# Performance work log

Hardware: AMD Instinct MI355X
Metric: run time of the kernel (lower is better)

## Reference

```python
import jax, jax.numpy as jnp
import numpy as np

# hyperparameters (from init_kwargs / repo defaults)
AMP_COEF = 1.0
ARG_COEF = 1.0
SSIM_COEF = 1.0
BETA = 1.0
STFT_COEF = 1e-4
EPS = 1e-8
STFT_F = 12
STFT_S = 4


def _gauss_kernel(size=11, sigma=1.5):
    x = jnp.arange(size, dtype=jnp.float32) - (size - 1) / 2.0
    g = jnp.exp(-0.5 * (x / sigma) ** 2)
    k = jnp.outer(g, g)
    return k / jnp.sum(k)


def _depthwise_filter(img, k):
    # img: [B,H,W,C]; 11x11 gaussian, VALID padding, depthwise (per-channel)
    c = img.shape[-1]
    kern = jnp.tile(k[:, :, None, None], (1, 1, 1, c))  # HWIO, I=1, O=C
    return jax.lax.conv_general_dilated(
        img, kern, (1, 1), 'VALID',
        dimension_numbers=('NHWC', 'HWIO', 'NHWC'),
        feature_group_count=c)


def ssim(x, y, max_val=1.0):
    # faithful to tf.image.ssim defaults: filter 11, sigma 1.5, k1=0.01, k2=0.03
    c1 = (0.01 * max_val) ** 2
    c2 = (0.03 * max_val) ** 2
    k = _gauss_kernel()
    mu_x = _depthwise_filter(x, k)
    mu_y = _depthwise_filter(y, k)
    var_x = _depthwise_filter(x * x, k) - mu_x * mu_x
    var_y = _depthwise_filter(y * y, k) - mu_y * mu_y
    cov = _depthwise_filter(x * y, k) - mu_x * mu_y
    lum = (2.0 * mu_x * mu_y + c1) / (mu_x * mu_x + mu_y * mu_y + c1)
    cs = (2.0 * cov + c2) / (var_x + var_y + c2)
    return jnp.mean(lum * cs, axis=(1, 2, 3))  # [B]


def stft(image, f=STFT_F, s=STFT_S):
    # image: [B,N,N,C] -> batched patchwise 2D FFT, cropped to [:f//2,:f//2]
    n = image.shape[1]
    p = (n - f) // s + 1          # num_conv per axis
    half = f // 2
    rows = (jnp.arange(p) * s)[:, None] + jnp.arange(f)   # [P, f]
    patches = image[:, rows]                              # [B,P,f,N,C]
    patches = patches[:, :, :, rows]                      # [B,P,f,P,f,C]
    patches = jnp.transpose(patches, (0, 1, 3, 2, 4, 5))  # [B,Pi,Pj,f,f,C]
    b, c = image.shape[0], image.shape[-1]
    patches = patches.reshape(b, p * p, f, f, c)          # k = i*P + j ordering
    fft = jnp.fft.fft2(patches.astype(jnp.complex64), axes=(2, 3))
    return fft[:, :, :half, :half, :]                     # [B,P*P,half,half,C]


def _freq_filter(f=STFT_F):
    lin = jnp.linspace(0.0, 1.0, f // 2)[:, None]
    return (lin * lin.T)[:, :, None]                      # [half,half,1]


def setup_inputs() -> dict:
    key = jax.random.key(0)
    k1, k2, k3, k4 = jax.random.split(key, 4)
    B, N, C, L = 32, 160, 3, 128
    return {
        'mean': jax.random.normal(k1, (B, L), dtype=jnp.float32),
        'logvar': jax.random.normal(k2, (B, L), dtype=jnp.float32),
        'x_in': jax.random.uniform(k3, (B, N, N, C), dtype=jnp.float32),
        'x_out': jax.random.uniform(k4, (B, N, N, C), dtype=jnp.float32),
    }


def reference(mean, logvar, x_in, x_out):
    # KLD per sample
    var = jnp.exp(logvar)
    kld = -0.5 * jnp.sum(1.0 + logvar - var - mean * mean, axis=1)  # [B]
    # SSIM recon term
    recons = SSIM_COEF * ssim(x_in, x_out, 1.0)                     # [B]
    # patchwise STFT amp/phase loss ('ours')
    stft_out = stft(x_out, STFT_F, STFT_S)
    stft_in = stft(x_in, STFT_F, STFT_S)
    ff = _freq_filter(STFT_F)                                       # [half,half,1]
    arg_diff = jnp.abs(jnp.angle(stft_out + EPS) - jnp.angle(stft_in + EPS))
    amp_diff = jnp.abs(jnp.abs(stft_out) - jnp.abs(stft_in))
    arg_loss = jnp.sum(arg_diff * ff, axis=(1, 2, 3, 4))            # [B]
    amp_loss = jnp.sum(amp_diff * ff, axis=(1, 2, 3, 4))            # [B]
    stft_loss = ARG_COEF * arg_loss + AMP_COEF * amp_loss
    loss = jnp.mean(BETA * kld + recons + STFT_COEF * stft_loss)
    return loss
```

## Files before the change

kernel.cpp:

```cpp
#include <hip/hip_runtime.h>
#include <hip/hip_fp16.h>
#include <math.h>

#define BATCH 32
#define NPIX 160
#define LDIM 128
#define OUT_SZ 150

#define THREADS 512
#define N_BLOCKS 1825
#define SCRATCH_OFF 2880
#define VSTRIDE 1296
#define SMEM_FLOATS 9360

__device__ constexpr float TWC[12] = { 1.f, 0.86602540f, 0.5f, 0.f, -0.5f, -0.86602540f,
                                      -1.f,-0.86602540f,-0.5f, 0.f,  0.5f,  0.86602540f};
__device__ constexpr float TWS[12] = { 0.f,-0.5f,-0.86602540f,-1.f,-0.86602540f,-0.5f,
                                       0.f, 0.5f, 0.86602540f, 1.f, 0.86602540f, 0.5f};

__device__ constexpr float GW[11] = {0.00102838f, 0.00759876f, 0.03600076f, 0.10936070f,
                                     0.21300554f, 0.26601172f, 0.21300554f, 0.10936070f,
                                     0.03600076f, 0.00759876f, 0.00102838f};

__device__ __forceinline__ float fast_atan2f(float y, float x) {
    float ax = fabsf(x), ay = fabsf(y);
    float mx = fmaxf(ax, ay), mn = fminf(ax, ay);
    float z = mn / mx;
    float z2 = z * z;
    float p = fmaf(z2, -0.01172120f, 0.05265332f);
    p = fmaf(z2, p, -0.11643287f);
    p = fmaf(z2, p, 0.19354346f);
    p = fmaf(z2, p, -0.33262347f);
    p = fmaf(z2, p, 0.99997726f);
    p = p * z;
    if (ay > ax) p = 1.57079632679489662f - p;
    if (x < 0.f) p = 3.14159265358979323f - p;
    return (y < 0.f) ? -p : p;
}

__device__ __forceinline__ float4 extract_c(float4 f0, float4 f1, float4 f2, int c) {
    if (c == 0) return make_float4(f0.x, f0.w, f1.z, f2.y);
    if (c == 1) return make_float4(f0.y, f1.x, f1.w, f2.z);
    return make_float4(f0.z, f1.y, f2.x, f2.w);
}

__global__ __launch_bounds__(THREADS) void work_kernel(const float* __restrict__ xin,
                                                       const float* __restrict__ xout,
                                                       const float* __restrict__ mean,
                                                       const float* __restrict__ logvar,
                                                       float* __restrict__ out) {
    __shared__ __align__(16) float SMEM[SMEM_FLOATS];
    __shared__ float sm8[8];
    const int tid = threadIdx.x;
    const int gid = blockIdx.x;
    float acc = 0.f;

    if (gid == 1824) {
        float a = 0.f;
        for (int i = tid; i < BATCH * LDIM; i += THREADS) {
            float m = mean[i], lv = logvar[i];
            a += -0.5f * (1.f + lv - expf(lv) - m * m) * (1.f / 32.f);
        }
        #pragma unroll
        for (int o = 32; o > 0; o >>= 1) a += __shfl_down(a, o, 64);
        if ((tid & 63) == 0) sm8[tid >> 6] = a;
        __syncthreads();
        if (tid == 0) {
            float s = sm8[0];
            #pragma unroll
            for (int i = 1; i < 8; ++i) s += sm8[i];
            atomicAdd(out, s);
        }
        return;
    }

    int b    = gid / 57;
    int rem  = gid % 57;
    int c    = rem / 19;
    int tile = rem % 19;
    int r0 = tile * 8;
    __half2* HXY = (__half2*)SMEM;
    __half2* RD  = (__half2*)(SMEM + SCRATCH_OFF);

    for (int t = tid; t < 720; t += THREADS) {
        int rr = t / 40;
        int cq = t % 40;
        int row = r0 + rr;
        float4 xa = make_float4(0.f, 0.f, 0.f, 0.f);
        float4 xb = make_float4(0.f, 0.f, 0.f, 0.f);
        if (row < NPIX) {
            size_t off = ((size_t)(b * 160 + row) * 160 + cq * 4) * 3;
            const float4* qa = (const float4*)(xin + off);
            const float4* qb = (const float4*)(xout + off);
            float4 a0 = qa[0], a1 = qa[1], a2 = qa[2];
            float4 b0 = qb[0], b1 = qb[1], b2 = qb[2];
            xa = extract_c(a0, a1, a2, c);
            xb = extract_c(b0, b1, b2, c);
        }
        __half2 h[4] __attribute__((aligned(16)));
        h[0] = __floats2half2_rn(xa.x, xb.x);
        h[1] = __floats2half2_rn(xa.y, xb.y);
        h[2] = __floats2half2_rn(xa.z, xb.z);
        h[3] = __floats2half2_rn(xa.w, xb.w);
        *(float4*)&HXY[rr * 160 + cq * 4] = *(float4*)h;
    }
    __syncthreads();

    for (int t = tid; t < 608; t += THREADS) {
        int pc = t % 38;
        int r  = t / 38;
        float4 raw[3];
        raw[0] = *(const float4*)&HXY[r * 160 + pc * 4];
        raw[1] = *(const float4*)&HXY[r * 160 + pc * 4 + 4];
        raw[2] = *(const float4*)&HXY[r * 160 + pc * 4 + 8];
        const __half2* hp = (const __half2*)raw;
        float xa[12], xb[12];
        #pragma unroll
        for (int j = 0; j < 12; ++j) {
            float2 xy = __half22float2(hp[j]);
            xa[j] = xy.x; xb[j] = xy.y;
        }
        #pragma unroll
        for (int img = 0; img < 2; ++img) {
            const float* x = img ? xb : xa;
            float ev[5] = {x[1]+x[11], x[2]+x[10], x[3]+x[9], x[4]+x[8], x[5]+x[7]};
            float ov[5] = {x[1]-x[11], x[2]-x[10], x[3]-x[9], x[4]-x[8], x[5]-x[7]};
            #pragma unroll
            for (int vv = 0; vv < 5; ++vv) {
                int v = vv + 1;
                float re = x[0] + ((v & 1) ? -x[6] : x[6]);
                float im = 0.f;
                #pragma unroll
                for (int j = 1; j <= 5; ++j) {
                    int kk = (v * j) % 12;
                    re = fmaf(ev[j-1], TWC[kk], re);
                    im = fmaf(ov[j-1], TWS[kk], im);
                }
                RD[((r * 5 + vv) * 2 + img) * 38 + pc] = __floats2half2_rn(re, im);
            }
        }
    }
    __syncthreads();

    if (tid < 380) {
        int pc = tid % 38;
        int vv = (tid / 38) % 5;
        int g  = tid / 190;
        float FR0[5] = {0,0,0,0,0}, FI0[5] = {0,0,0,0,0};
        float FR1[5] = {0,0,0,0,0}, FI1[5] = {0,0,0,0,0};
        #pragma unroll
        for (int i = 0; i < 6; ++i) {
            int rlo = 4 * g + i, rhi = rlo + 6;
            float2 a0 = __half22float2(RD[((rlo * 5 + vv) * 2 + 0) * 38 + pc]);
            float2 a6 = __half22float2(RD[((rhi * 5 + vv) * 2 + 0) * 38 + pc]);
            float2 b0 = __half22float2(RD[((rlo * 5 + vv) * 2 + 1) * 38 + pc]);
            float2 b6 = __half22float2(RD[((rhi * 5 + vv) * 2 + 1) * 38 + pc]);
            float spR0 = a0.x + a6.x, spI0 = a0.y + a6.y;
            float smR0 = a0.x - a6.x, smI0 = a0.y - a6.y;
            float spR1 = b0.x + b6.x, spI1 = b0.y + b6.y;
            float smR1 = b0.x - b6.x, smI1 = b0.y - b6.y;
            #pragma unroll
            for (int uu = 0; uu < 5; ++uu) {
                int u = uu + 1;
                int kk = (u * i) % 12;
                float cu = TWC[kk], su = TWS[kk];
                float sR0 = (u & 1) ? smR0 : spR0, sI0 = (u & 1) ? smI0 : spI0;
                float sR1 = (u & 1) ? smR1 : spR1, sI1 = (u & 1) ? smI1 : spI1;
                FR0[uu] = fmaf(cu, sR0, fmaf(-su, sI0, FR0[uu]));
                FI0[uu] = fmaf(cu, sI0, fmaf( su, sR0, FI0[uu]));
                FR1[uu] = fmaf(cu, sR1, fmaf(-su, sI1, FR1[uu]));
                FI1[uu] = fmaf(cu, sI1, fmaf( su, sR1, FI1[uu]));
            }
        }
        float sacc = 0.f;
        #pragma unroll
        for (int uu = 0; uu < 5; ++uu) {
            float aI = fast_atan2f(FI0[uu], FR0[uu] + 1e-8f);
            float aO = fast_atan2f(FI1[uu], FR1[uu] + 1e-8f);
            float mI = sqrtf(FR0[uu] * FR0[uu] + FI0[uu] * FI0[uu]);
            float mO = sqrtf(FR1[uu] * FR1[uu] + FI1[uu] * FI1[uu]);
            float ff = (float)((uu + 1) * (vv + 1)) * 0.04f;
            sacc += ff * (fabsf(aO - aI) + fabsf(mO - mI));
        }
        acc += sacc * (1e-4f / 32.f);
    }
    __syncthreads();

    for (int t = tid; t < 320; t += THREADS) {
        int orow = t / 40;
        int cbase = (t % 40) * 4;
        float ax[4] = {0,0,0,0}, ay[4] = {0,0,0,0};
        float axx[4] = {0,0,0,0}, ayy[4] = {0,0,0,0}, axy[4] = {0,0,0,0};
        #pragma unroll
        for (int kk = 0; kk < 11; ++kk) {
            float4 raw = *(const float4*)&HXY[(orow + kk) * 160 + cbase];
            const __half2* hp = (const __half2*)&raw;
            float wg = GW[kk];
            #pragma unroll
            for (int o = 0; o < 4; ++o) {
                float2 xy = __half22float2(hp[o]);
                ax[o]  += wg * xy.x;          ay[o]  += wg * xy.y;
                axx[o] += wg * (xy.x * xy.x); ayy[o] += wg * (xy.y * xy.y);
                axy[o] += wg * (xy.x * xy.y);
            }
        }
        int base = SCRATCH_OFF + orow * 160 + cbase;
        *(float4*)&SMEM[base + 0 * VSTRIDE] = make_float4(ax[0],  ax[1],  ax[2],  ax[3]);
        *(float4*)&SMEM[base + 1 * VSTRIDE] = make_float4(ay[0],  ay[1],  ay[2],  ay[3]);
        *(float4*)&SMEM[base + 2 * VSTRIDE] = make_float4(axx[0], axx[1], axx[2], axx[3]);
        *(float4*)&SMEM[base + 3 * VSTRIDE] = make_float4(ayy[0], ayy[1], ayy[2], ayy[3]);
        *(float4*)&SMEM[base + 4 * VSTRIDE] = make_float4(axy[0], axy[1], axy[2], axy[3]);
    }
    __syncthreads();

    {
        float hacc = 0.f;
        for (int t = tid; t < 600; t += THREADS) {
            int orow = t / 75;
            int oc = (t % 75) * 2;
            float st[5][2];
            #pragma unroll
            for (int p = 0; p < 5; ++p) {
                float vals[12];
                #pragma unroll
                for (int kk = 0; kk < 12; ++kk)
                    vals[kk] = SMEM[SCRATCH_OFF + p * VSTRIDE + orow * 160 + oc + kk];
                float s0 = 0.f, s1 = 0.f;
                #pragma unroll
                for (int kk = 0; kk < 11; ++kk) {
                    s0 += GW[kk] * vals[kk];
                    s1 += GW[kk] * vals[kk + 1];
                }
                st[p][0] = s0; st[p][1] = s1;
            }
            const float c1 = 1e-4f, c2 = 9e-4f;
            if (r0 + orow < OUT_SZ) {
                #pragma unroll
                for (int o = 0; o < 2; ++o) {
                    float mx = st[0][o], my = st[1][o];
                    float vx = st[2][o] - mx * mx;
                    float vy = st[3][o] - my * my;
                    float cv = st[4][o] - mx * my;
                    float lum = (2.f * mx * my + c1) / (mx * mx + my * my + c1);
                    float cs  = (2.f * cv + c2) / (vx + vy + c2);
                    hacc += lum * cs;
                }
            }
        }
        acc += hacc * (1.f / (32.f * 150.f * 150.f * 3.f));
    }

    #pragma unroll
    for (int o = 32; o > 0; o >>= 1) acc += __shfl_down(acc, o, 64);
    if ((tid & 63) == 0) sm8[tid >> 6] = acc;
    __syncthreads();
    if (tid == 0) {
        float s = sm8[0];
        #pragma unroll
        for (int i = 1; i < 8; ++i) s += sm8[i];
        atomicAdd(out, s);
    }
}

extern "C" void kernel_launch(void* const* d_in, const int* in_sizes, int n_in,
                              void* d_out, int out_size, void* d_ws, size_t ws_size,
                              hipStream_t stream) {
    const float* mean   = (const float*)d_in[0];
    const float* logvar = (const float*)d_in[1];
    const float* xin    = (const float*)d_in[2];
    const float* xout   = (const float*)d_in[3];
    float* out = (float*)d_out;

    hipMemsetAsync(out, 0, sizeof(float), stream);
    work_kernel<<<N_BLOCKS, THREADS, 0, stream>>>(xin, xout, mean, logvar, out);
}
```

Measured before the change: 122.6 us.

## Use fast rcp/sqrt intrinsics, interleave RD layout, vectorize LDS loads

Replaces IEEE divisions and sqrt with the hardware rcp/sqrt intrinsics in atan2, SSIM and the magnitude computation. It also interleaves the two images' row-DFT results in the RD buffer so each is written and read as one 8-byte access, and loads the horizontal-pass values as float2. The separable-filter accumulation is rewritten with FMAs. The approximate intrinsics give up a little accuracy in exchange for fewer instructions and fewer LDS transactions.

```diff
diff --git a/kernel.cpp b/kernel.cpp
--- a/kernel.cpp
+++ b/kernel.cpp
@@ -25,7 +25,7 @@
 __device__ __forceinline__ float fast_atan2f(float y, float x) {
     float ax = fabsf(x), ay = fabsf(y);
     float mx = fmaxf(ax, ay), mn = fminf(ax, ay);
-    float z = mn / mx;
+    float z = mn * __builtin_amdgcn_rcpf(mx);
     float z2 = z * z;
     float p = fmaf(z2, -0.01172120f, 0.05265332f);
     p = fmaf(z2, p, -0.11643287f);
@@ -120,24 +120,28 @@
             float2 xy = __half22float2(hp[j]);
             xa[j] = xy.x; xb[j] = xy.y;
         }
-        #pragma unroll
-        for (int img = 0; img < 2; ++img) {
-            const float* x = img ? xb : xa;
-            float ev[5] = {x[1]+x[11], x[2]+x[10], x[3]+x[9], x[4]+x[8], x[5]+x[7]};
-            float ov[5] = {x[1]-x[11], x[2]-x[10], x[3]-x[9], x[4]-x[8], x[5]-x[7]};
-            #pragma unroll
-            for (int vv = 0; vv < 5; ++vv) {
-                int v = vv + 1;
-                float re = x[0] + ((v & 1) ? -x[6] : x[6]);
-                float im = 0.f;
-                #pragma unroll
-                for (int j = 1; j <= 5; ++j) {
-                    int kk = (v * j) % 12;
-                    re = fmaf(ev[j-1], TWC[kk], re);
-                    im = fmaf(ov[j-1], TWS[kk], im);
-                }
-                RD[((r * 5 + vv) * 2 + img) * 38 + pc] = __floats2half2_rn(re, im);
-            }
+        float evA[5] = {xa[1]+xa[11], xa[2]+xa[10], xa[3]+xa[9], xa[4]+xa[8], xa[5]+xa[7]};
+        float ovA[5] = {xa[1]-xa[11], xa[2]-xa[10], xa[3]-xa[9], xa[4]-xa[8], xa[5]-xa[7]};
+        float evB[5] = {xb[1]+xb[11], xb[2]+xb[10], xb[3]+xb[9], xb[4]+xb[8], xb[5]+xb[7]};
+        float ovB[5] = {xb[1]-xb[11], xb[2]-xb[10], xb[3]-xb[9], xb[4]-xb[8], xb[5]-xb[7]};
+        #pragma unroll
+        for (int vv = 0; vv < 5; ++vv) {
+            int v = vv + 1;
+            float reA = xa[0] + ((v & 1) ? -xa[6] : xa[6]);
+            float reB = xb[0] + ((v & 1) ? -xb[6] : xb[6]);
+            float imA = 0.f, imB = 0.f;
+            #pragma unroll
+            for (int j = 1; j <= 5; ++j) {
+                int kk = (v * j) % 12;
+                reA = fmaf(evA[j-1], TWC[kk], reA);
+                imA = fmaf(ovA[j-1], TWS[kk], imA);
+                reB = fmaf(evB[j-1], TWC[kk], reB);
+                imB = fmaf(ovB[j-1], TWS[kk], imB);
+            }
+            __half2 w2[2] __attribute__((aligned(8)));
+            w2[0] = __floats2half2_rn(reA, imA);
+            w2[1] = __floats2half2_rn(reB, imB);
+            *(float2*)&RD[(((r * 5 + vv) * 38) + pc) * 2] = *(float2*)w2;
         }
     }
     __syncthreads();
@@ -151,10 +155,14 @@
         #pragma unroll
         for (int i = 0; i < 6; ++i) {
             int rlo = 4 * g + i, rhi = rlo + 6;
-            float2 a0 = __half22float2(RD[((rlo * 5 + vv) * 2 + 0) * 38 + pc]);
-            float2 a6 = __half22float2(RD[((rhi * 5 + vv) * 2 + 0) * 38 + pc]);
-            float2 b0 = __half22float2(RD[((rlo * 5 + vv) * 2 + 1) * 38 + pc]);
-            float2 b6 = __half22float2(RD[((rhi * 5 + vv) * 2 + 1) * 38 + pc]);
+            __half2 p0[2] __attribute__((aligned(8)));
+            __half2 p6[2] __attribute__((aligned(8)));
+            *(float2*)p0 = *(const float2*)&RD[(((rlo * 5 + vv) * 38) + pc) * 2];
+            *(float2*)p6 = *(const float2*)&RD[(((rhi * 5 + vv) * 38) + pc) * 2];
+            float2 a0 = __half22float2(p0[0]);
+            float2 b0 = __half22float2(p0[1]);
+            float2 a6 = __half22float2(p6[0]);
+            float2 b6 = __half22float2(p6[1]);
             float spR0 = a0.x + a6.x, spI0 = a0.y + a6.y;
             float smR0 = a0.x - a6.x, smI0 = a0.y - a6.y;
             float spR1 = b0.x + b6.x, spI1 = b0.y + b6.y;
@@ -177,8 +185,8 @@
         for (int uu = 0; uu < 5; ++uu) {
             float aI = fast_atan2f(FI0[uu], FR0[uu] + 1e-8f);
             float aO = fast_atan2f(FI1[uu], FR1[uu] + 1e-8f);
-            float mI = sqrtf(FR0[uu] * FR0[uu] + FI0[uu] * FI0[uu]);
-            float mO = sqrtf(FR1[uu] * FR1[uu] + FI1[uu] * FI1[uu]);
+            float mI = __builtin_amdgcn_sqrtf(fmaf(FR0[uu], FR0[uu], FI0[uu] * FI0[uu]));
+            float mO = __builtin_amdgcn_sqrtf(fmaf(FR1[uu], FR1[uu], FI1[uu] * FI1[uu]));
             float ff = (float)((uu + 1) * (vv + 1)) * 0.04f;
             sacc += ff * (fabsf(aO - aI) + fabsf(mO - mI));
         }
@@ -199,9 +207,12 @@
             #pragma unroll
             for (int o = 0; o < 4; ++o) {
                 float2 xy = __half22float2(hp[o]);
-                ax[o]  += wg * xy.x;          ay[o]  += wg * xy.y;
-                axx[o] += wg * (xy.x * xy.x); ayy[o] += wg * (xy.y * xy.y);
-                axy[o] += wg * (xy.x * xy.y);
+                float tx = wg * xy.x, ty = wg * xy.y;
+                ax[o]  += tx;
+                ay[o]  += ty;
+                axx[o] = fmaf(tx, xy.x, axx[o]);
+                ayy[o] = fmaf(ty, xy.y, ayy[o]);
+                axy[o] = fmaf(tx, xy.y, axy[o]);
             }
         }
         int base = SCRATCH_OFF + orow * 160 + cbase;
@@ -221,10 +232,14 @@
             float st[5][2];
             #pragma unroll
             for (int p = 0; p < 5; ++p) {
+                const float* rowp = &SMEM[SCRATCH_OFF + p * VSTRIDE + orow * 160 + oc];
                 float vals[12];
                 #pragma unroll
-                for (int kk = 0; kk < 12; ++kk)
-                    vals[kk] = SMEM[SCRATCH_OFF + p * VSTRIDE + orow * 160 + oc + kk];
+                for (int q = 0; q < 6; ++q) {
+                    float2 v2 = *(const float2*)&rowp[2 * q];
+                    vals[2 * q]     = v2.x;
+                    vals[2 * q + 1] = v2.y;
+                }
                 float s0 = 0.f, s1 = 0.f;
                 #pragma unroll
                 for (int kk = 0; kk < 11; ++kk) {
@@ -241,8 +256,10 @@
                     float vx = st[2][o] - mx * mx;
                     float vy = st[3][o] - my * my;
                     float cv = st[4][o] - mx * my;
-                    float lum = (2.f * mx * my + c1) / (mx * mx + my * my + c1);
-                    float cs  = (2.f * cv + c2) / (vx + vy + c2);
+                    float lum = (2.f * mx * my + c1) *
+                                __builtin_amdgcn_rcpf(fmaf(mx, mx, my * my) + c1);
+                    float cs  = (2.f * cv + c2) *
+                                __builtin_amdgcn_rcpf(vx + vy + c2);
                     hacc += lum * cs;
                 }
             }
```

New measurement: 116.9 us. 1.05x faster.
